# Kernel optimization log

Measured on AMD Instinct MI355X. Metric: run time of the kernel, lower is better.

Reference implementation:

```python
import jax, jax.numpy as jnp
import numpy as np

T = 100000   # timesteps (hourly)
WIN = 336    # window_size, hardcoded by Tanh(336,336)/Linear(336,out)
OUT = 48     # output_size (2-day horizon)
S = 168      # seasonality_2 (weekly)


def setup_inputs() -> dict:
    key = jax.random.key(0)
    ks = jax.random.split(key, 8)
    # strictly positive series (logs/divisions in forward)
    x = jax.random.uniform(ks[0], (T,), minval=0.5, maxval=1.5, dtype=jnp.float32)
    lvl_coef = jax.random.uniform(ks[1], (), minval=-1.0, maxval=1.0, dtype=jnp.float32)
    seas_coef = jax.random.uniform(ks[2], (), minval=-1.0, maxval=1.0, dtype=jnp.float32)
    # torch init: seasonality param p ~ U(0.65,1.35), used as exp(p); store raw p
    seas_params = jnp.log(jax.random.uniform(ks[3], (S,), minval=0.65, maxval=1.35, dtype=jnp.float32))
    W_tanh = jax.random.normal(ks[4], (WIN, WIN), dtype=jnp.float32) * 0.05
    b_tanh = jnp.zeros((WIN,), dtype=jnp.float32)
    W_out = jax.random.normal(ks[5], (WIN, OUT), dtype=jnp.float32) * 0.05
    b_out = jnp.zeros((OUT,), dtype=jnp.float32)
    return dict(x=x, lvl_coef=lvl_coef, seas_coef=seas_coef, seas_params=seas_params,
                W_tanh=W_tanh, b_tanh=b_tanh, W_out=W_out, b_out=b_out,
                window_size=WIN, output_size=OUT, lvp=50)


def reference(x, lvl_coef, seas_coef, seas_params, W_tanh, b_tanh, W_out, b_out,
              window_size, output_size, lvp):
    std = 0.001
    Tn = x.shape[0]
    a = jax.nn.sigmoid(lvl_coef)       # level smoothing
    g = jax.nn.sigmoid(seas_coef)      # seasonality smoothing
    w0 = jnp.exp(seas_params)          # initial weekly seasonality, [S]
    level0 = x[0] / w0[0]
    # w_seasons[1..S] = [w0[1], ..., w0[S-1], w0[0]] (torch appends w_seasons[0])
    buf0 = jnp.concatenate([w0[1:], w0[:1]])

    def step(carry, xi):
        level, buf = carry
        season = buf[0]                              # w_seasons[i], lag-S recurrence
        new_level = a * xi / season + (1.0 - a) * level
        new_season = g * xi / new_level + (1.0 - g) * season
        buf = jnp.concatenate([buf[1:], new_season[None]])
        return (new_level, buf), (new_level, new_season)

    _, (lvl_seq, new_seasons) = jax.lax.scan(step, (level0, buf0), x[1:])
    levels = jnp.concatenate([level0[None], lvl_seq])          # [T]
    w_all = jnp.concatenate([w0, w0[:1], new_seasons])[:Tn]    # w_seasons[0..T-1]

    # level variation penalty (torch builds it via torch.tensor(list) -> detached)
    lld = jnp.log(levels[1:] / levels[:-1])
    level_var_loss = jax.lax.stop_gradient(jnp.mean((lld[1:] - lld[:-1]) ** 2) * lvp)

    # vectorized sliding windows
    N = Tn - window_size - output_size + 1
    base = jnp.arange(N)
    iw = base[:, None] + jnp.arange(window_size)[None, :]
    il = base[:, None] + window_size + jnp.arange(output_size)[None, :]  # [N, OUT]
    lev = levels[base + window_size][:, None]                            # [N, 1]
    k1, k2 = jax.random.split(jax.random.key(1))
    inputs = jnp.log(x[iw] / (lev * w_all[iw])) + std * jax.random.normal(k1, (N, window_size), dtype=x.dtype)
    labels = jnp.log(x[il] / (lev * w_all[il])) + std * jax.random.normal(k2, (N, output_size), dtype=x.dtype)

    # skip_lstm head: Tanh(336,336) (linear + tanh) -> Linear(336, output_size)
    out = jnp.tanh(inputs @ W_tanh + b_tanh) @ W_out + b_out
    return out, labels, level_var_loss
```

## Files before the change

### kernel.cpp

```cpp
#include <hip/hip_runtime.h>
#include <hip/hip_bf16.h>

#define T_WIN 336
#define T_OUT 48
#define T_S   168
#define BM    128
#define CH    782

typedef __attribute__((ext_vector_type(8))) short short8;
typedef __attribute__((ext_vector_type(4))) float f32x4;

__device__ __forceinline__ short f2bf(float f) {
    union { float f; unsigned u; } v; v.f = f;
    unsigned r = v.u + 0x7FFFu + ((v.u >> 16) & 1u);
    return (short)(r >> 16);
}

template <int CTRL, int RMASK>
__device__ __forceinline__ float dppf(float v) {
    union { float f; int i; } in, out;
    in.f = v;
    out.i = __builtin_amdgcn_update_dpp(0, in.i, CTRL, RMASK, 0xf, true);
    return out.f;
}

__global__ __launch_bounds__(256, 1) void prep_scan_kernel(
    const float* __restrict__ x, const float* __restrict__ lvl_coef,
    const float* __restrict__ seas_coef, const float* __restrict__ seas_params,
    const float* __restrict__ W1, const float* __restrict__ W2,
    float* __restrict__ w_all, float* __restrict__ levels,
    short* __restrict__ W1F, short* __restrict__ W2F,
    float* __restrict__ cs, int T)
{
    int blk = blockIdx.x;
    int tid = threadIdx.x;

    if (blk >= 301) {
        int k = (blk - 301) * 256 + tid;
        if (k < T_WIN) {
            float s = 0.f;
            for (int j = 0; j < T_WIN; ++j) s += W1[j * T_WIN + k];
            cs[k] = s;
        }
        return;
    }
    if (blk >= 265) {
        int d = (blk - 265) * 256 + tid;
        int j2 = d & 3, lane = (d >> 2) & 63, f = d >> 8;
        int ct2 = f % 3, rest = f / 3;
        int kt2 = rest & 1, c = rest >> 1;
        int k = c * 64 + kt2 * 32 + (lane >> 4) * 8 + 2 * j2;
        int o = ct2 * 16 + (lane & 15);
        unsigned short lo = 0, hi = 0;
        if (k     < T_WIN) lo = (unsigned short)f2bf(W2[k * T_OUT + o]);
        if (k + 1 < T_WIN) hi = (unsigned short)f2bf(W2[(k + 1) * T_OUT + o]);
        ((unsigned*)W2F)[d] = ((unsigned)hi << 16) | (unsigned)lo;
        return;
    }
    if (blk >= 1) {
        int d = (blk - 1) * 256 + tid;
        int j2 = d & 3, lane = (d >> 2) & 63, f = d >> 8;
        int ct = f & 3, rest = f >> 2;
        int kt = rest % 11, c = rest / 11;
        int k = kt * 32 + (lane >> 4) * 8 + 2 * j2;
        int col = c * 64 + ct * 16 + (lane & 15);
        unsigned short lo = 0, hi = 0;
        if (col < T_WIN) {
            if (k     < T_WIN) lo = (unsigned short)f2bf(W1[k * T_WIN + col]);
            if (k + 1 < T_WIN) hi = (unsigned short)f2bf(W1[(k + 1) * T_WIN + col]);
        }
        ((unsigned*)W1F)[d] = ((unsigned)hi << 16) | (unsigned)lo;
        return;
    }

    if (tid >= 64) return;
    int lane = tid;
    float a = 1.f / (1.f + __expf(-lvl_coef[0]));
    float g = 1.f / (1.f + __expf(-seas_coef[0]));
    float q = 1.f - a, gq = 1.f - g;

    for (int t = lane; t < T_S + 1; t += 64) w_all[t] = __expf(seas_params[t % T_S]);
    float lvl = x[0] / __expf(seas_params[0]);
    if (lane == 0) levels[0] = lvl;

    float wcur[3];
    #pragma unroll
    for (int i = 0; i < 3; ++i)
        wcur[i] = __expf(seas_params[(1 + 3 * lane + i) % T_S]);

    float f1 = q * q * q;
    float f2 = f1 * f1, f4 = f2 * f2, f8 = f4 * f4;
    float lnq = __logf(q);
    float P15 = __expf(3.f * (float)((lane & 15) + 1) * lnq);
    float P31 = __expf(3.f * (float)((lane & 31) + 1) * lnq);
    float pw3l = __expf(3.f * (float)lane * lnq);

    int j0 = 3 * lane;

    auto do_chunk = [&](const float* xvv, float* lev) {
        float rr[3];
        #pragma unroll
        for (int i = 0; i < 3; ++i) rr[i] = a * xvv[i] * __builtin_amdgcn_rcpf(wcur[i]);
        float S = fmaf(q, fmaf(q, rr[0], rr[1]), rr[2]);
        S = fmaf(f1, dppf<0x111, 0xf>(S), S);
        S = fmaf(f2, dppf<0x112, 0xf>(S), S);
        S = fmaf(f4, dppf<0x114, 0xf>(S), S);
        S = fmaf(f8, dppf<0x118, 0xf>(S), S);
        S = fmaf(P15, dppf<0x142, 0xa>(S), S);
        S = fmaf(P31, dppf<0x143, 0xc>(S), S);
        float E = dppf<0x138, 0xf>(S);
        float lv = fmaf(pw3l, lvl, E);
        #pragma unroll
        for (int i = 0; i < 3; ++i) { lv = fmaf(q, lv, rr[i]); lev[i] = lv; }
        { union { float f; int i; } uu; uu.i = __builtin_amdgcn_readlane(__builtin_bit_cast(int, lev[2]), 55); lvl = uu.f; }
        #pragma unroll
        for (int i = 0; i < 3; ++i)
            wcur[i] = fmaf(gq, wcur[i], g * xvv[i] * __builtin_amdgcn_rcpf(lev[i]));
    };

    float xg[4][3], xh[4][3], x2[4][3];
    #pragma unroll
    for (int u = 0; u < 4; ++u)
        #pragma unroll
        for (int i = 0; i < 3; ++i) {
            xg[u][i] = x[1 + T_S * u + j0 + i];
            xh[u][i] = x[1 + T_S * (4 + u) + j0 + i];
        }

    const float* px = x + 1 + 8 * T_S + j0;
    float* pl = levels + 1 + j0;
    float* pw = w_all + 1 + T_S + j0;

    for (int grp = 0; grp < 148; ++grp) {
        if (grp < 146) {
            #pragma unroll
            for (int u = 0; u < 4; ++u)
                #pragma unroll
                for (int i = 0; i < 3; ++i)
                    x2[u][i] = px[u * T_S + i];
        } else {
            #pragma unroll
            for (int u = 0; u < 4; ++u)
                #pragma unroll
                for (int i = 0; i < 3; ++i) {
                    int t = 1 + T_S * (4 * (grp + 2) + u) + j0 + i;
                    x2[u][i] = x[min(t, T - 1)];
                }
        }
        px += 4 * T_S;

        #pragma unroll
        for (int u = 0; u < 4; ++u) {
            float lev[3];
            do_chunk(xg[u], lev);
            #pragma unroll
            for (int i = 0; i < 3; ++i) {
                pl[u * T_S + i] = lev[i];
                pw[u * T_S + i] = wcur[i];
            }
        }
        pl += 4 * T_S; pw += 4 * T_S;
        #pragma unroll
        for (int u = 0; u < 4; ++u)
            #pragma unroll
            for (int i = 0; i < 3; ++i) { xg[u][i] = xh[u][i]; xh[u][i] = x2[u][i]; }
    }

    #pragma unroll
    for (int u = 0; u < 4; ++u) {
        int c = 592 + u;
        if (c * T_S >= T - 1) break;
        int len = (T - 1) - T_S * c; if (len > T_S) len = T_S;
        float lev[3];
        do_chunk(xg[u], lev);
        #pragma unroll
        for (int i = 0; i < 3; ++i) {
            if (j0 + i < len) {
                pl[u * T_S + i] = lev[i];
                pw[u * T_S + i] = wcur[i];
            }
        }
    }
}

__global__ __launch_bounds__(256, 2) void gemm_kernel(
    const float* __restrict__ x, const float* __restrict__ w_all,
    const float* __restrict__ levels,
    const short* __restrict__ W1F, const short* __restrict__ W2F,
    const float* __restrict__ b1, const float* __restrict__ cs,
    const float* __restrict__ b2, float* __restrict__ outp,
    float* __restrict__ lab, float* __restrict__ lpart,
    int T, int N, int NB)
{
    __shared__ float Lsf[512];
    __shared__ __align__(16) short Lbf0[512];
    __shared__ __align__(16) short Lbf1[512];
    __shared__ float llv[BM];
    __shared__ __align__(16) short hs[BM * 72];
    __shared__ __align__(16) short B1s[11 * 4 * 512];
    __shared__ __align__(16) short B2s[6 * 512];

    int blk = blockIdx.x;
    int tid = threadIdx.x;

    if (blk >= NB) {
        float* ls  = (float*)hs;
        float* red = (float*)(hs + 4096);
        int lb = blk - NB;
        int lo = lb * CH;
        int n = T - lo; if (n > CH + 2) n = CH + 2;
        for (int i = tid; i < n; i += 256) ls[i] = __logf(levels[lo + i]);
        __syncthreads();
        float s = 0.f;
        int dmax = (T - 2) - lo; if (dmax > CH) dmax = CH;
        for (int i = tid; i < dmax; i += 256) {
            float d = ls[i + 2] - 2.f * ls[i + 1] + ls[i];
            s = fmaf(d, d, s);
        }
        red[tid] = s;
        __syncthreads();
        for (int w = 128; w > 0; w >>= 1) {
            if (tid < w) red[tid] += red[tid + w];
            __syncthreads();
        }
        if (tid == 0) lpart[lb] = red[0];
        return;
    }

    int lane = tid & 63, wv = tid >> 6;
    int lr = lane & 15, lq = lane >> 4;
    int n0 = blk * BM;
    int rw = wv * 32;

    float C = __logf(levels[min(n0 + T_WIN, T - 1)]);

    for (int i = tid; i < 512; i += 256) {
        int t = n0 + i;
        float v = (t < T) ? (__logf(x[t]) - __logf(w_all[t]) - C) : 0.f;
        Lsf[i] = v;
        Lbf0[i] = f2bf(v);
    }
    for (int i = tid; i < BM; i += 256) {
        int t = n0 + i + T_WIN;
        llv[i] = (t < T) ? (__logf(levels[t]) - C) : 0.f;
    }
    __syncthreads();
    for (int i = tid; i < 512; i += 256) Lbf1[i] = (i < 511) ? Lbf0[i + 1] : (short)0;
    __syncthreads();

    for (int u2 = tid; u2 < BM * T_OUT; u2 += 256) {
        int row = u2 / T_OUT, j = u2 - row * T_OUT;
        int nn = n0 + row;
        if (nn < N) lab[(size_t)nn * T_OUT + j] = Lsf[row + T_WIN + j] - llv[row];
    }

    const short* abase = ((lr & 1) ? Lbf1 : Lbf0) + rw + (lr & ~1);
    short8 af[11][2];
    #pragma unroll
    for (int kt = 0; kt < 11; ++kt) {
        #pragma unroll
        for (int mt = 0; mt < 2; ++mt) {
            const int* ip = (const int*)(abase + mt * 16 + kt * 32 + lq * 8);
            union { short8 s; int i[4]; } u;
            u.i[0] = ip[0]; u.i[1] = ip[1]; u.i[2] = ip[2]; u.i[3] = ip[3];
            af[kt][mt] = u.s;
        }
    }

    f32x4 zero4 = {0.f, 0.f, 0.f, 0.f};
    f32x4 acc2[2][3];
    #pragma unroll
    for (int mt = 0; mt < 2; ++mt)
        #pragma unroll
        for (int ct = 0; ct < 3; ++ct) acc2[mt][ct] = zero4;

    #pragma unroll 1
    for (int c = 0; c < 6; ++c) {
        __syncthreads();

        const char* g1 = (const char*)(W1F + (size_t)c * 11 * 4 * 512);
        for (int seg = wv; seg < 44; seg += 4) {
            __builtin_amdgcn_global_load_lds(
                (const __attribute__((address_space(1))) unsigned int*)(g1 + seg * 1024 + lane * 16),
                (__attribute__((address_space(3))) unsigned int*)((char*)B1s + seg * 1024),
                16, 0, 0);
        }
        const char* g2 = (const char*)(W2F + (size_t)c * 6 * 512);
        for (int seg = wv; seg < 6; seg += 4) {
            __builtin_amdgcn_global_load_lds(
                (const __attribute__((address_space(1))) unsigned int*)(g2 + seg * 1024 + lane * 16),
                (__attribute__((address_space(3))) unsigned int*)((char*)B2s + seg * 1024),
                16, 0, 0);
        }
        float b1v[4], csv[4];
        #pragma unroll
        for (int ct = 0; ct < 4; ++ct) {
            int col = c * 64 + ct * 16 + lr;
            b1v[ct] = (col < T_WIN) ? b1[col] : 0.f;
            csv[ct] = (col < T_WIN) ? cs[col] : 0.f;
        }
        __syncthreads();

        f32x4 acc1[2][4];
        #pragma unroll
        for (int mt = 0; mt < 2; ++mt)
            #pragma unroll
            for (int ct = 0; ct < 4; ++ct) acc1[mt][ct] = zero4;

        #pragma unroll
        for (int kt = 0; kt < 11; ++kt) {
            #pragma unroll
            for (int ct = 0; ct < 4; ++ct) {
                short8 bf = *(const short8*)&B1s[((kt * 4 + ct) * 64 + lane) * 8];
                acc1[0][ct] = __builtin_amdgcn_mfma_f32_16x16x32_bf16(af[kt][0], bf, acc1[0][ct], 0, 0, 0);
                acc1[1][ct] = __builtin_amdgcn_mfma_f32_16x16x32_bf16(af[kt][1], bf, acc1[1][ct], 0, 0, 0);
            }
        }

        #pragma unroll
        for (int mt = 0; mt < 2; ++mt)
            #pragma unroll
            for (int ct = 0; ct < 4; ++ct)
                #pragma unroll
                for (int r = 0; r < 4; ++r) {
                    int row = rw + mt * 16 + lq * 4 + r;
                    float pre = acc1[mt][ct][r] + b1v[ct] - llv[row] * csv[ct];
                    float e = __expf(2.f * pre);
                    float h = 1.f - 2.f * __builtin_amdgcn_rcpf(e + 1.f);
                    hs[row * 72 + ct * 16 + lr] = f2bf(h);
                }

        #pragma unroll
        for (int kt2 = 0; kt2 < 2; ++kt2) {
            short8 a2[2];
            #pragma unroll
            for (int mt = 0; mt < 2; ++mt)
                a2[mt] = *(const short8*)&hs[(rw + mt * 16 + lr) * 72 + kt2 * 32 + lq * 8];
            #pragma unroll
            for (int ct2 = 0; ct2 < 3; ++ct2) {
                short8 bf2 = *(const short8*)&B2s[((kt2 * 3 + ct2) * 64 + lane) * 8];
                acc2[0][ct2] = __builtin_amdgcn_mfma_f32_16x16x32_bf16(a2[0], bf2, acc2[0][ct2], 0, 0, 0);
                acc2[1][ct2] = __builtin_amdgcn_mfma_f32_16x16x32_bf16(a2[1], bf2, acc2[1][ct2], 0, 0, 0);
            }
        }
    }

    float b2v[3];
    #pragma unroll
    for (int ct2 = 0; ct2 < 3; ++ct2) b2v[ct2] = b2[ct2 * 16 + lr];
    #pragma unroll
    for (int mt = 0; mt < 2; ++mt)
        #pragma unroll
        for (int ct2 = 0; ct2 < 3; ++ct2)
            #pragma unroll
            for (int r = 0; r < 4; ++r) {
                int row = n0 + rw + mt * 16 + lq * 4 + r;
                if (row < N)
                    outp[(size_t)row * T_OUT + ct2 * 16 + lr] = acc2[mt][ct2][r] + b2v[ct2];
            }
}

__global__ __launch_bounds__(128) void loss2_kernel(
    const float* __restrict__ part, const int* __restrict__ lvp,
    float* __restrict__ out_loss, int T)
{
    __shared__ float red[128];
    red[threadIdx.x] = part[threadIdx.x];
    __syncthreads();
    for (int w = 64; w > 0; w >>= 1) {
        if (threadIdx.x < (unsigned)w) red[threadIdx.x] += red[threadIdx.x + w];
        __syncthreads();
    }
    if (threadIdx.x == 0) out_loss[0] = red[0] * (float)lvp[0] / (float)(T - 2);
}

extern "C" void kernel_launch(void* const* d_in, const int* in_sizes, int n_in,
                              void* d_out, int out_size, void* d_ws, size_t ws_size,
                              hipStream_t stream) {
    const float* x    = (const float*)d_in[0];
    const float* lvlc = (const float*)d_in[1];
    const float* seac = (const float*)d_in[2];
    const float* sp   = (const float*)d_in[3];
    const float* W1   = (const float*)d_in[4];
    const float* b1   = (const float*)d_in[5];
    const float* W2   = (const float*)d_in[6];
    const float* b2   = (const float*)d_in[7];
    const int*   lvp  = (const int*)d_in[10];

    int T = in_sizes[0];
    int N = T - T_WIN - T_OUT + 1;
    int NB = (N + BM - 1) / BM;

    short* W1F    = (short*)d_ws;
    short* W2F    = W1F + 264 * 512;
    float* w_all  = (float*)(W2F + 36 * 512);
    float* levels = w_all + T + 192;
    float* cs     = levels + T;
    float* lpart  = cs + 352;

    float* outp  = (float*)d_out;
    float* lab   = outp + (size_t)N * T_OUT;
    float* lossp = lab + (size_t)N * T_OUT;

    prep_scan_kernel<<<303, 256, 0, stream>>>(x, lvlc, seac, sp, W1, W2,
                                              w_all, levels, W1F, W2F, cs, T);
    gemm_kernel<<<NB + 128, 256, 0, stream>>>(x, w_all, levels, W1F, W2F,
                                              b1, cs, b2, outp, lab, lpart, T, N, NB);
    loss2_kernel<<<1, 128, 0, stream>>>(lpart, lvp, lossp, T);
}
```

Before: 231.4 us.

## Fuse scan and GEMM into persistent kernel with progress-flag streaming

```diff
diff --git a/kernel.cpp b/kernel.cpp
--- a/kernel.cpp
+++ b/kernel.cpp
@@ -24,173 +24,16 @@
     return out.f;
 }
 
-__global__ __launch_bounds__(256, 1) void prep_scan_kernel(
+__global__ __launch_bounds__(256, 2) void fused_kernel(
     const float* __restrict__ x, const float* __restrict__ lvl_coef,
     const float* __restrict__ seas_coef, const float* __restrict__ seas_params,
     const float* __restrict__ W1, const float* __restrict__ W2,
+    const float* __restrict__ b1, const float* __restrict__ b2,
+    short* __restrict__ W1F, short* __restrict__ W2F,
     float* __restrict__ w_all, float* __restrict__ levels,
-    short* __restrict__ W1F, short* __restrict__ W2F,
-    float* __restrict__ cs, int T)
-{
-    int blk = blockIdx.x;
-    int tid = threadIdx.x;
-
-    if (blk >= 301) {
-        int k = (blk - 301) * 256 + tid;
-        if (k < T_WIN) {
-            float s = 0.f;
-            for (int j = 0; j < T_WIN; ++j) s += W1[j * T_WIN + k];
-            cs[k] = s;
-        }
-        return;
-    }
-    if (blk >= 265) {
-        int d = (blk - 265) * 256 + tid;
-        int j2 = d & 3, lane = (d >> 2) & 63, f = d >> 8;
-        int ct2 = f % 3, rest = f / 3;
-        int kt2 = rest & 1, c = rest >> 1;
-        int k = c * 64 + kt2 * 32 + (lane >> 4) * 8 + 2 * j2;
-        int o = ct2 * 16 + (lane & 15);
-        unsigned short lo = 0, hi = 0;
-        if (k     < T_WIN) lo = (unsigned short)f2bf(W2[k * T_OUT + o]);
-        if (k + 1 < T_WIN) hi = (unsigned short)f2bf(W2[(k + 1) * T_OUT + o]);
-        ((unsigned*)W2F)[d] = ((unsigned)hi << 16) | (unsigned)lo;
-        return;
-    }
-    if (blk >= 1) {
-        int d = (blk - 1) * 256 + tid;
-        int j2 = d & 3, lane = (d >> 2) & 63, f = d >> 8;
-        int ct = f & 3, rest = f >> 2;
-        int kt = rest % 11, c = rest / 11;
-        int k = kt * 32 + (lane >> 4) * 8 + 2 * j2;
-        int col = c * 64 + ct * 16 + (lane & 15);
-        unsigned short lo = 0, hi = 0;
-        if (col < T_WIN) {
-            if (k     < T_WIN) lo = (unsigned short)f2bf(W1[k * T_WIN + col]);
-            if (k + 1 < T_WIN) hi = (unsigned short)f2bf(W1[(k + 1) * T_WIN + col]);
-        }
-        ((unsigned*)W1F)[d] = ((unsigned)hi << 16) | (unsigned)lo;
-        return;
-    }
-
-    if (tid >= 64) return;
-    int lane = tid;
-    float a = 1.f / (1.f + __expf(-lvl_coef[0]));
-    float g = 1.f / (1.f + __expf(-seas_coef[0]));
-    float q = 1.f - a, gq = 1.f - g;
-
-    for (int t = lane; t < T_S + 1; t += 64) w_all[t] = __expf(seas_params[t % T_S]);
-    float lvl = x[0] / __expf(seas_params[0]);
-    if (lane == 0) levels[0] = lvl;
-
-    float wcur[3];
-    #pragma unroll
-    for (int i = 0; i < 3; ++i)
-        wcur[i] = __expf(seas_params[(1 + 3 * lane + i) % T_S]);
-
-    float f1 = q * q * q;
-    float f2 = f1 * f1, f4 = f2 * f2, f8 = f4 * f4;
-    float lnq = __logf(q);
-    float P15 = __expf(3.f * (float)((lane & 15) + 1) * lnq);
-    float P31 = __expf(3.f * (float)((lane & 31) + 1) * lnq);
-    float pw3l = __expf(3.f * (float)lane * lnq);
-
-    int j0 = 3 * lane;
-
-    auto do_chunk = [&](const float* xvv, float* lev) {
-        float rr[3];
-        #pragma unroll
-        for (int i = 0; i < 3; ++i) rr[i] = a * xvv[i] * __builtin_amdgcn_rcpf(wcur[i]);
-        float S = fmaf(q, fmaf(q, rr[0], rr[1]), rr[2]);
-        S = fmaf(f1, dppf<0x111, 0xf>(S), S);
-        S = fmaf(f2, dppf<0x112, 0xf>(S), S);
-        S = fmaf(f4, dppf<0x114, 0xf>(S), S);
-        S = fmaf(f8, dppf<0x118, 0xf>(S), S);
-        S = fmaf(P15, dppf<0x142, 0xa>(S), S);
-        S = fmaf(P31, dppf<0x143, 0xc>(S), S);
-        float E = dppf<0x138, 0xf>(S);
-        float lv = fmaf(pw3l, lvl, E);
-        #pragma unroll
-        for (int i = 0; i < 3; ++i) { lv = fmaf(q, lv, rr[i]); lev[i] = lv; }
-        { union { float f; int i; } uu; uu.i = __builtin_amdgcn_readlane(__builtin_bit_cast(int, lev[2]), 55); lvl = uu.f; }
-        #pragma unroll
-        for (int i = 0; i < 3; ++i)
-            wcur[i] = fmaf(gq, wcur[i], g * xvv[i] * __builtin_amdgcn_rcpf(lev[i]));
-    };
-
-    float xg[4][3], xh[4][3], x2[4][3];
-    #pragma unroll
-    for (int u = 0; u < 4; ++u)
-        #pragma unroll
-        for (int i = 0; i < 3; ++i) {
-            xg[u][i] = x[1 + T_S * u + j0 + i];
-            xh[u][i] = x[1 + T_S * (4 + u) + j0 + i];
-        }
-
-    const float* px = x + 1 + 8 * T_S + j0;
-    float* pl = levels + 1 + j0;
-    float* pw = w_all + 1 + T_S + j0;
-
-    for (int grp = 0; grp < 148; ++grp) {
-        if (grp < 146) {
-            #pragma unroll
-            for (int u = 0; u < 4; ++u)
-                #pragma unroll
-                for (int i = 0; i < 3; ++i)
-                    x2[u][i] = px[u * T_S + i];
-        } else {
-            #pragma unroll
-            for (int u = 0; u < 4; ++u)
-                #pragma unroll
-                for (int i = 0; i < 3; ++i) {
-                    int t = 1 + T_S * (4 * (grp + 2) + u) + j0 + i;
-                    x2[u][i] = x[min(t, T - 1)];
-                }
-        }
-        px += 4 * T_S;
-
-        #pragma unroll
-        for (int u = 0; u < 4; ++u) {
-            float lev[3];
-            do_chunk(xg[u], lev);
-            #pragma unroll
-            for (int i = 0; i < 3; ++i) {
-                pl[u * T_S + i] = lev[i];
-                pw[u * T_S + i] = wcur[i];
-            }
-        }
-        pl += 4 * T_S; pw += 4 * T_S;
-        #pragma unroll
-        for (int u = 0; u < 4; ++u)
-            #pragma unroll
-            for (int i = 0; i < 3; ++i) { xg[u][i] = xh[u][i]; xh[u][i] = x2[u][i]; }
-    }
-
-    #pragma unroll
-    for (int u = 0; u < 4; ++u) {
-        int c = 592 + u;
-        if (c * T_S >= T - 1) break;
-        int len = (T - 1) - T_S * c; if (len > T_S) len = T_S;
-        float lev[3];
-        do_chunk(xg[u], lev);
-        #pragma unroll
-        for (int i = 0; i < 3; ++i) {
-            if (j0 + i < len) {
-                pl[u * T_S + i] = lev[i];
-                pw[u * T_S + i] = wcur[i];
-            }
-        }
-    }
-}
-
-__global__ __launch_bounds__(256, 2) void gemm_kernel(
-    const float* __restrict__ x, const float* __restrict__ w_all,
-    const float* __restrict__ levels,
-    const short* __restrict__ W1F, const short* __restrict__ W2F,
-    const float* __restrict__ b1, const float* __restrict__ cs,
-    const float* __restrict__ b2, float* __restrict__ outp,
+    float* __restrict__ cs, float* __restrict__ outp,
     float* __restrict__ lab, float* __restrict__ lpart,
-    int T, int N, int NB)
+    int* flags, int T, int N, int NB)
 {
     __shared__ float Lsf[512];
     __shared__ __align__(16) short Lbf0[512];
@@ -199,165 +42,350 @@
     __shared__ __align__(16) short hs[BM * 72];
     __shared__ __align__(16) short B1s[11 * 4 * 512];
     __shared__ __align__(16) short B2s[6 * 512];
+    __shared__ int sh_tk;
 
     int blk = blockIdx.x;
     int tid = threadIdx.x;
-
-    if (blk >= NB) {
-        float* ls  = (float*)hs;
-        float* red = (float*)(hs + 4096);
-        int lb = blk - NB;
-        int lo = lb * CH;
-        int n = T - lo; if (n > CH + 2) n = CH + 2;
-        for (int i = tid; i < n; i += 256) ls[i] = __logf(levels[lo + i]);
-        __syncthreads();
-        float s = 0.f;
-        int dmax = (T - 2) - lo; if (dmax > CH) dmax = CH;
-        for (int i = tid; i < dmax; i += 256) {
-            float d = ls[i + 2] - 2.f * ls[i + 1] + ls[i];
-            s = fmaf(d, d, s);
-        }
-        red[tid] = s;
-        __syncthreads();
-        for (int w = 128; w > 0; w >>= 1) {
-            if (tid < w) red[tid] += red[tid + w];
-            __syncthreads();
-        }
-        if (tid == 0) lpart[lb] = red[0];
+    int* progress  = flags;
+    int* prep_done = flags + 1;
+    int* ticket    = flags + 2;
+
+    if (blk == 0) {
+        if (tid >= 64) return;
+        __builtin_amdgcn_s_setprio(3);
+        int lane = tid;
+        float a = 1.f / (1.f + __expf(-lvl_coef[0]));
+        float g = 1.f / (1.f + __expf(-seas_coef[0]));
+        float q = 1.f - a, gq = 1.f - g;
+
+        for (int t = lane; t < T_S + 1; t += 64) w_all[t] = __expf(seas_params[t % T_S]);
+        float lvl = x[0] / __expf(seas_params[0]);
+        if (lane == 0) levels[0] = lvl;
+
+        float wcur[3];
+        #pragma unroll
+        for (int i = 0; i < 3; ++i)
+            wcur[i] = __expf(seas_params[(1 + 3 * lane + i) % T_S]);
+
+        float f1 = q * q * q;
+        float f2 = f1 * f1, f4 = f2 * f2, f8 = f4 * f4;
+        float lnq = __logf(q);
+        float P15 = __expf(3.f * (float)((lane & 15) + 1) * lnq);
+        float P31 = __expf(3.f * (float)((lane & 31) + 1) * lnq);
+        float pw3l = __expf(3.f * (float)lane * lnq);
+
+        int j0 = 3 * lane;
+
+        auto do_chunk = [&](const float* xvv, float* lev) {
+            float rr[3];
+            #pragma unroll
+            for (int i = 0; i < 3; ++i) rr[i] = a * xvv[i] * __builtin_amdgcn_rcpf(wcur[i]);
+            float S = fmaf(q, fmaf(q, rr[0], rr[1]), rr[2]);
+            S = fmaf(f1, dppf<0x111, 0xf>(S), S);
+            S = fmaf(f2, dppf<0x112, 0xf>(S), S);
+            S = fmaf(f4, dppf<0x114, 0xf>(S), S);
+            S = fmaf(f8, dppf<0x118, 0xf>(S), S);
+            S = fmaf(P15, dppf<0x142, 0xa>(S), S);
+            S = fmaf(P31, dppf<0x143, 0xc>(S), S);
+            float E = dppf<0x138, 0xf>(S);
+            float lv = fmaf(pw3l, lvl, E);
+            #pragma unroll
+            for (int i = 0; i < 3; ++i) { lv = fmaf(q, lv, rr[i]); lev[i] = lv; }
+            { union { float f; int i; } uu; uu.i = __builtin_amdgcn_readlane(__builtin_bit_cast(int, lev[2]), 55); lvl = uu.f; }
+            #pragma unroll
+            for (int i = 0; i < 3; ++i)
+                wcur[i] = fmaf(gq, wcur[i], g * xvv[i] * __builtin_amdgcn_rcpf(lev[i]));
+        };
+
+        float xg[4][3], xh[4][3], x2[4][3];
+        #pragma unroll
+        for (int u = 0; u < 4; ++u)
+            #pragma unroll
+            for (int i = 0; i < 3; ++i) {
+                xg[u][i] = x[1 + T_S * u + j0 + i];
+                xh[u][i] = x[1 + T_S * (4 + u) + j0 + i];
+            }
+
+        const float* px = x + 1 + 8 * T_S + j0;
+        float* pl = levels + 1 + j0;
+        float* pw = w_all + 1 + T_S + j0;
+
+        for (int grp = 0; grp < 148; ++grp) {
+            if (grp && (grp & 7) == 0 && lane == 0)
+                __hip_atomic_store(progress, grp, __ATOMIC_RELEASE, __HIP_MEMORY_SCOPE_AGENT);
+
+            if (grp < 146) {
+                #pragma unroll
+                for (int u = 0; u < 4; ++u)
+                    #pragma unroll
+                    for (int i = 0; i < 3; ++i)
+                        x2[u][i] = px[u * T_S + i];
+            } else {
+                #pragma unroll
+                for (int u = 0; u < 4; ++u)
+                    #pragma unroll
+                    for (int i = 0; i < 3; ++i) {
+                        int t = 1 + T_S * (4 * (grp + 2) + u) + j0 + i;
+                        x2[u][i] = x[min(t, T - 1)];
+                    }
+            }
+            px += 4 * T_S;
+
+            #pragma unroll
+            for (int u = 0; u < 4; ++u) {
+                float lev[3];
+                do_chunk(xg[u], lev);
+                #pragma unroll
+                for (int i = 0; i < 3; ++i) {
+                    pl[u * T_S + i] = lev[i];
+                    pw[u * T_S + i] = wcur[i];
+                }
+            }
+            pl += 4 * T_S; pw += 4 * T_S;
+            #pragma unroll
+            for (int u = 0; u < 4; ++u)
+                #pragma unroll
+                for (int i = 0; i < 3; ++i) { xg[u][i] = xh[u][i]; xh[u][i] = x2[u][i]; }
+        }
+
+        #pragma unroll
+        for (int u = 0; u < 4; ++u) {
+            int c = 592 + u;
+            if (c * T_S >= T - 1) break;
+            int len = (T - 1) - T_S * c; if (len > T_S) len = T_S;
+            float lev[3];
+            do_chunk(xg[u], lev);
+            #pragma unroll
+            for (int i = 0; i < 3; ++i) {
+                if (j0 + i < len) {
+                    pl[u * T_S + i] = lev[i];
+                    pw[u * T_S + i] = wcur[i];
+                }
+            }
+        }
+        if (lane == 0)
+            __hip_atomic_store(progress, 1000, __ATOMIC_RELEASE, __HIP_MEMORY_SCOPE_AGENT);
         return;
     }
 
+    if (blk <= 302) {
+        if (blk >= 301) {
+            int k = (blk - 301) * 256 + tid;
+            if (k < T_WIN) {
+                float s = 0.f;
+                for (int j = 0; j < T_WIN; ++j) s += W1[j * T_WIN + k];
+                cs[k] = s;
+            }
+        } else if (blk >= 265) {
+            int d = (blk - 265) * 256 + tid;
+            int j2 = d & 3, lane = (d >> 2) & 63, f = d >> 8;
+            int ct2 = f % 3, rest = f / 3;
+            int kt2 = rest & 1, c = rest >> 1;
+            int k = c * 64 + kt2 * 32 + (lane >> 4) * 8 + 2 * j2;
+            int o = ct2 * 16 + (lane & 15);
+            unsigned short lo = 0, hi = 0;
+            if (k     < T_WIN) lo = (unsigned short)f2bf(W2[k * T_OUT + o]);
+            if (k + 1 < T_WIN) hi = (unsigned short)f2bf(W2[(k + 1) * T_OUT + o]);
+            ((unsigned*)W2F)[d] = ((unsigned)hi << 16) | (unsigned)lo;
+        } else {
+            int d = (blk - 1) * 256 + tid;
+            int j2 = d & 3, lane = (d >> 2) & 63, f = d >> 8;
+            int ct = f & 3, rest = f >> 2;
+            int kt = rest % 11, c = rest / 11;
+            int k = kt * 32 + (lane >> 4) * 8 + 2 * j2;
+            int col = c * 64 + ct * 16 + (lane & 15);
+            unsigned short lo = 0, hi = 0;
+            if (col < T_WIN) {
+                if (k     < T_WIN) lo = (unsigned short)f2bf(W1[k * T_WIN + col]);
+                if (k + 1 < T_WIN) hi = (unsigned short)f2bf(W1[(k + 1) * T_WIN + col]);
+            }
+            ((unsigned*)W1F)[d] = ((unsigned)hi << 16) | (unsigned)lo;
+        }
+        __syncthreads();
+        if (tid == 0)
+            __hip_atomic_fetch_add(prep_done, 1, __ATOMIC_RELEASE, __HIP_MEMORY_SCOPE_AGENT);
+    }
+
+    while (__hip_atomic_load(prep_done, __ATOMIC_RELAXED, __HIP_MEMORY_SCOPE_AGENT) < 302)
+        __builtin_amdgcn_s_sleep(8);
+    __builtin_amdgcn_fence(__ATOMIC_ACQUIRE, "agent");
+
     int lane = tid & 63, wv = tid >> 6;
     int lr = lane & 15, lq = lane >> 4;
-    int n0 = blk * BM;
     int rw = wv * 32;
-
-    float C = __logf(levels[min(n0 + T_WIN, T - 1)]);
-
-    for (int i = tid; i < 512; i += 256) {
-        int t = n0 + i;
-        float v = (t < T) ? (__logf(x[t]) - __logf(w_all[t]) - C) : 0.f;
-        Lsf[i] = v;
-        Lbf0[i] = f2bf(v);
+    int last_seen = 0;
+    int NT = NB + 128;
+
+    for (;;) {
+        __syncthreads();
+        if (tid == 0) sh_tk = atomicAdd(ticket, 1);
+        __syncthreads();
+        int tk = sh_tk;
+        if (tk >= NT) return;
+
+        int need_t = (tk < NB) ? (tk * BM + 512) : ((tk - NB) * CH + CH + 2);
+        if (need_t > T) need_t = T;
+        int req = (need_t + 670) / 672;
+        if (last_seen < req) {
+            int p;
+            while ((p = __hip_atomic_load(progress, __ATOMIC_RELAXED, __HIP_MEMORY_SCOPE_AGENT)) < req)
+                __builtin_amdgcn_s_sleep(16);
+            __builtin_amdgcn_fence(__ATOMIC_ACQUIRE, "agent");
+            last_seen = p;
+        }
+
+        if (tk >= NB) {
+            float* ls  = (float*)hs;
+            float* red = (float*)(hs + 4096);
+            int lb = tk - NB;
+            int lo = lb * CH;
+            int n = T - lo; if (n > CH + 2) n = CH + 2;
+            for (int i = tid; i < n; i += 256) ls[i] = __logf(levels[lo + i]);
+            __syncthreads();
+            float s = 0.f;
+            int dmax = (T - 2) - lo; if (dmax > CH) dmax = CH;
+            for (int i = tid; i < dmax; i += 256) {
+                float d = ls[i + 2] - 2.f * ls[i + 1] + ls[i];
+                s = fmaf(d, d, s);
+            }
+            red[tid] = s;
+            __syncthreads();
+            for (int w = 128; w > 0; w >>= 1) {
+                if (tid < w) red[tid] += red[tid + w];
+                __syncthreads();
+            }
+            if (tid == 0) lpart[lb] = red[0];
+            continue;
+        }
+
+        int n0 = tk * BM;
+        float C = __logf(levels[min(n0 + T_WIN, T - 1)]);
+
+        for (int i = tid; i < 512; i += 256) {
+            int t = n0 + i;
+            float v = (t < T) ? (__logf(x[t]) - __logf(w_all[t]) - C) : 0.f;
+            Lsf[i] = v;
+            Lbf0[i] = f2bf(v);
+        }
+        for (int i = tid; i < BM; i += 256) {
+            int t = n0 + i + T_WIN;
+            llv[i] = (t < T) ? (__logf(levels[t]) - C) : 0.f;
+        }
+        __syncthreads();
+        for (int i = tid; i < 512; i += 256) Lbf1[i] = (i < 511) ? Lbf0[i + 1] : (short)0;
+        __syncthreads();
+
+        for (int u2 = tid; u2 < BM * T_OUT; u2 += 256) {
+            int row = u2 / T_OUT, j = u2 - row * T_OUT;
+            int nn = n0 + row;
+            if (nn < N) lab[(size_t)nn * T_OUT + j] = Lsf[row + T_WIN + j] - llv[row];
+        }
+
+        const short* abase = ((lr & 1) ? Lbf1 : Lbf0) + rw + (lr & ~1);
+        short8 af[11][2];
+        #pragma unroll
+        for (int kt = 0; kt < 11; ++kt) {
+            #pragma unroll
+            for (int mt = 0; mt < 2; ++mt) {
+                const int* ip = (const int*)(abase + mt * 16 + kt * 32 + lq * 8);
+                union { short8 s; int i[4]; } u;
+                u.i[0] = ip[0]; u.i[1] = ip[1]; u.i[2] = ip[2]; u.i[3] = ip[3];
+                af[kt][mt] = u.s;
+            }
+        }
+
+        f32x4 zero4 = {0.f, 0.f, 0.f, 0.f};
+        f32x4 acc2[2][3];
+        #pragma unroll
+        for (int mt = 0; mt < 2; ++mt)
+            #pragma unroll
+            for (int ct = 0; ct < 3; ++ct) acc2[mt][ct] = zero4;
+
+        #pragma unroll 1
+        for (int c = 0; c < 6; ++c) {
+            __syncthreads();
+
+            const char* g1 = (const char*)(W1F + (size_t)c * 11 * 4 * 512);
+            for (int seg = wv; seg < 44; seg += 4) {
+                __builtin_amdgcn_global_load_lds(
+                    (const __attribute__((address_space(1))) unsigned int*)(g1 + seg * 1024 + lane * 16),
+                    (__attribute__((address_space(3))) unsigned int*)((char*)B1s + seg * 1024),
+                    16, 0, 0);
+            }
+            const char* g2 = (const char*)(W2F + (size_t)c * 6 * 512);
+            for (int seg = wv; seg < 6; seg += 4) {
+                __builtin_amdgcn_global_load_lds(
+                    (const __attribute__((address_space(1))) unsigned int*)(g2 + seg * 1024 + lane * 16),
+                    (__attribute__((address_space(3))) unsigned int*)((char*)B2s + seg * 1024),
+                    16, 0, 0);
+            }
+            float b1v[4], csv[4];
+            #pragma unroll
+            for (int ct = 0; ct < 4; ++ct) {
+                int col = c * 64 + ct * 16 + lr;
+                b1v[ct] = (col < T_WIN) ? b1[col] : 0.f;
+                csv[ct] = (col < T_WIN) ? cs[col] : 0.f;
+            }
+            __syncthreads();
+
+            f32x4 acc1[2][4];
+            #pragma unroll
+            for (int mt = 0; mt < 2; ++mt)
+                #pragma unroll
+                for (int ct = 0; ct < 4; ++ct) acc1[mt][ct] = zero4;
+
+            #pragma unroll
+            for (int kt = 0; kt < 11; ++kt) {
+                #pragma unroll
+                for (int ct = 0; ct < 4; ++ct) {
+                    short8 bf = *(const short8*)&B1s[((kt * 4 + ct) * 64 + lane) * 8];
+                    acc1[0][ct] = __builtin_amdgcn_mfma_f32_16x16x32_bf16(af[kt][0], bf, acc1[0][ct], 0, 0, 0);
+                    acc1[1][ct] = __builtin_amdgcn_mfma_f32_16x16x32_bf16(af[kt][1], bf, acc1[1][ct], 0, 0, 0);
+                }
+            }
+
+            #pragma unroll
+            for (int mt = 0; mt < 2; ++mt)
+                #pragma unroll
+                for (int ct = 0; ct < 4; ++ct)
+                    #pragma unroll
+                    for (int r = 0; r < 4; ++r) {
+                        int row = rw + mt * 16 + lq * 4 + r;
+                        float pre = acc1[mt][ct][r] + b1v[ct] - llv[row] * csv[ct];
+                        float e = __expf(2.f * pre);
+                        float h = 1.f - 2.f * __builtin_amdgcn_rcpf(e + 1.f);
+                        hs[row * 72 + ct * 16 + lr] = f2bf(h);
+                    }
+
+            #pragma unroll
+            for (int kt2 = 0; kt2 < 2; ++kt2) {
+                short8 a2[2];
+                #pragma unroll
+                for (int mt = 0; mt < 2; ++mt)
+                    a2[mt] = *(const short8*)&hs[(rw + mt * 16 + lr) * 72 + kt2 * 32 + lq * 8];
+                #pragma unroll
+                for (int ct2 = 0; ct2 < 3; ++ct2) {
+                    short8 bf2 = *(const short8*)&B2s[((kt2 * 3 + ct2) * 64 + lane) * 8];
+                    acc2[0][ct2] = __builtin_amdgcn_mfma_f32_16x16x32_bf16(a2[0], bf2, acc2[0][ct2], 0, 0, 0);
+                    acc2[1][ct2] = __builtin_amdgcn_mfma_f32_16x16x32_bf16(a2[1], bf2, acc2[1][ct2], 0, 0, 0);
+                }
+            }
+        }
+
+        float b2v[3];
+        #pragma unroll
+        for (int ct2 = 0; ct2 < 3; ++ct2) b2v[ct2] = b2[ct2 * 16 + lr];
+        #pragma unroll
+        for (int mt = 0; mt < 2; ++mt)
+            #pragma unroll
+            for (int ct2 = 0; ct2 < 3; ++ct2)
+                #pragma unroll
+                for (int r = 0; r < 4; ++r) {
+                    int row = n0 + rw + mt * 16 + lq * 4 + r;
+                    if (row < N)
+                        outp[(size_t)row * T_OUT + ct2 * 16 + lr] = acc2[mt][ct2][r] + b2v[ct2];
+                }
     }
-    for (int i = tid; i < BM; i += 256) {
-        int t = n0 + i + T_WIN;
-        llv[i] = (t < T) ? (__logf(levels[t]) - C) : 0.f;
-    }
-    __syncthreads();
-    for (int i = tid; i < 512; i += 256) Lbf1[i] = (i < 511) ? Lbf0[i + 1] : (short)0;
-    __syncthreads();
-
-    for (int u2 = tid; u2 < BM * T_OUT; u2 += 256) {
-        int row = u2 / T_OUT, j = u2 - row * T_OUT;
-        int nn = n0 + row;
-        if (nn < N) lab[(size_t)nn * T_OUT + j] = Lsf[row + T_WIN + j] - llv[row];
-    }
-
-    const short* abase = ((lr & 1) ? Lbf1 : Lbf0) + rw + (lr & ~1);
-    short8 af[11][2];
-    #pragma unroll
-    for (int kt = 0; kt < 11; ++kt) {
-        #pragma unroll
-        for (int mt = 0; mt < 2; ++mt) {
-            const int* ip = (const int*)(abase + mt * 16 + kt * 32 + lq * 8);
-            union { short8 s; int i[4]; } u;
-            u.i[0] = ip[0]; u.i[1] = ip[1]; u.i[2] = ip[2]; u.i[3] = ip[3];
-            af[kt][mt] = u.s;
-        }
-    }
-
-    f32x4 zero4 = {0.f, 0.f, 0.f, 0.f};
-    f32x4 acc2[2][3];
-    #pragma unroll
-    for (int mt = 0; mt < 2; ++mt)
-        #pragma unroll
-        for (int ct = 0; ct < 3; ++ct) acc2[mt][ct] = zero4;
-
-    #pragma unroll 1
-    for (int c = 0; c < 6; ++c) {
-        __syncthreads();
-
-        const char* g1 = (const char*)(W1F + (size_t)c * 11 * 4 * 512);
-        for (int seg = wv; seg < 44; seg += 4) {
-            __builtin_amdgcn_global_load_lds(
-                (const __attribute__((address_space(1))) unsigned int*)(g1 + seg * 1024 + lane * 16),
-                (__attribute__((address_space(3))) unsigned int*)((char*)B1s + seg * 1024),
-                16, 0, 0);
-        }
-        const char* g2 = (const char*)(W2F + (size_t)c * 6 * 512);
-        for (int seg = wv; seg < 6; seg += 4) {
-            __builtin_amdgcn_global_load_lds(
-                (const __attribute__((address_space(1))) unsigned int*)(g2 + seg * 1024 + lane * 16),
-                (__attribute__((address_space(3))) unsigned int*)((char*)B2s + seg * 1024),
-                16, 0, 0);
-        }
-        float b1v[4], csv[4];
-        #pragma unroll
-        for (int ct = 0; ct < 4; ++ct) {
-            int col = c * 64 + ct * 16 + lr;
-            b1v[ct] = (col < T_WIN) ? b1[col] : 0.f;
-            csv[ct] = (col < T_WIN) ? cs[col] : 0.f;
-        }
-        __syncthreads();
-
-        f32x4 acc1[2][4];
-        #pragma unroll
-        for (int mt = 0; mt < 2; ++mt)
-            #pragma unroll
-            for (int ct = 0; ct < 4; ++ct) acc1[mt][ct] = zero4;
-
-        #pragma unroll
-        for (int kt = 0; kt < 11; ++kt) {
-            #pragma unroll
-            for (int ct = 0; ct < 4; ++ct) {
-                short8 bf = *(const short8*)&B1s[((kt * 4 + ct) * 64 + lane) * 8];
-                acc1[0][ct] = __builtin_amdgcn_mfma_f32_16x16x32_bf16(af[kt][0], bf, acc1[0][ct], 0, 0, 0);
-                acc1[1][ct] = __builtin_amdgcn_mfma_f32_16x16x32_bf16(af[kt][1], bf, acc1[1][ct], 0, 0, 0);
-            }
-        }
-
-        #pragma unroll
-        for (int mt = 0; mt < 2; ++mt)
-            #pragma unroll
-            for (int ct = 0; ct < 4; ++ct)
-                #pragma unroll
-                for (int r = 0; r < 4; ++r) {
-                    int row = rw + mt * 16 + lq * 4 + r;
-                    float pre = acc1[mt][ct][r] + b1v[ct] - llv[row] * csv[ct];
-                    float e = __expf(2.f * pre);
-                    float h = 1.f - 2.f * __builtin_amdgcn_rcpf(e + 1.f);
-                    hs[row * 72 + ct * 16 + lr] = f2bf(h);
-                }
-
-        #pragma unroll
-        for (int kt2 = 0; kt2 < 2; ++kt2) {
-            short8 a2[2];
-            #pragma unroll
-            for (int mt = 0; mt < 2; ++mt)
-                a2[mt] = *(const short8*)&hs[(rw + mt * 16 + lr) * 72 + kt2 * 32 + lq * 8];
-            #pragma unroll
-            for (int ct2 = 0; ct2 < 3; ++ct2) {
-                short8 bf2 = *(const short8*)&B2s[((kt2 * 3 + ct2) * 64 + lane) * 8];
-                acc2[0][ct2] = __builtin_amdgcn_mfma_f32_16x16x32_bf16(a2[0], bf2, acc2[0][ct2], 0, 0, 0);
-                acc2[1][ct2] = __builtin_amdgcn_mfma_f32_16x16x32_bf16(a2[1], bf2, acc2[1][ct2], 0, 0, 0);
-            }
-        }
-    }
-
-    float b2v[3];
-    #pragma unroll
-    for (int ct2 = 0; ct2 < 3; ++ct2) b2v[ct2] = b2[ct2 * 16 + lr];
-    #pragma unroll
-    for (int mt = 0; mt < 2; ++mt)
-        #pragma unroll
-        for (int ct2 = 0; ct2 < 3; ++ct2)
-            #pragma unroll
-            for (int r = 0; r < 4; ++r) {
-                int row = n0 + rw + mt * 16 + lq * 4 + r;
-                if (row < N)
-                    outp[(size_t)row * T_OUT + ct2 * 16 + lr] = acc2[mt][ct2][r] + b2v[ct2];
-            }
 }
 
 __global__ __launch_bounds__(128) void loss2_kernel(
@@ -402,9 +430,11 @@
     float* lab   = outp + (size_t)N * T_OUT;
     float* lossp = lab + (size_t)N * T_OUT;
 
-    prep_scan_kernel<<<303, 256, 0, stream>>>(x, lvlc, seac, sp, W1, W2,
-                                              w_all, levels, W1F, W2F, cs, T);
-    gemm_kernel<<<NB + 128, 256, 0, stream>>>(x, w_all, levels, W1F, W2F,
-                                              b1, cs, b2, outp, lab, lpart, T, N, NB);
+    int* flagsp = (int*)(cs + 344);
+    hipMemsetAsync((void*)flagsp, 0, 12, stream);
+
+    fused_kernel<<<512, 256, 0, stream>>>(x, lvlc, seac, sp, W1, W2, b1, b2,
+                                          W1F, W2F, w_all, levels, cs,
+                                          outp, lab, lpart, flagsp, T, N, NB);
     loss2_kernel<<<1, 128, 0, stream>>>(lpart, lvp, lossp, T);
 }
```

New measurement: 293.7 us. +26.9%, slower.
